# Kernel tuning notes

Measured on AMD Instinct MI355X. Metric: run time of the kernel, lower is better.

The kernel has to match this reference:

```python
import jax, jax.numpy as jnp
import numpy as np

B, V_PREV, V_NEXT = 1, 16384, 65536
F_IN, F_OUT = 512, 256
NNZ_UP, N_EDGE = 65536, 524288
EPS = 1e-5


def batch_spmm(row, col, val, m, x):
    # sparse [m, n] (COO row/col/val) @ dense x [B, n, d] -> [B, m, d]
    contrib = val[None, :, None] * x[:, col, :]          # [B, nnz, d]
    return jnp.zeros((x.shape[0], m, x.shape[2]), x.dtype).at[:, row, :].add(contrib)


def batchnorm(x, g, b):
    # BatchNorm1d in training mode: stats over (batch, node) per channel
    mu = jnp.mean(x, axis=(0, 1), keepdims=True)
    var = jnp.var(x, axis=(0, 1), keepdims=True)
    return (x - mu) * jax.lax.rsqrt(var + EPS) * g + b


def ecc(x, src, dst, w, Ui_W, Ui_b, Uj_W, Uj_b):
    # edge-conditioned graph conv: out_i = Ui(x_i) + sum_{(j->i)} w_e * Uj(x_j)
    n_nodes = x.shape[1]
    uj = x @ Uj_W + Uj_b                                  # [B, V, Fout]
    msg = w[None, :, None] * uj[:, src, :]                # [B, E, Fout]
    agg = jnp.zeros((x.shape[0], n_nodes, Uj_W.shape[1]), x.dtype).at[:, dst, :].add(msg)
    return x @ Ui_W + Ui_b + agg


def setup_inputs() -> dict:
    key = jax.random.key(0)
    ks = jax.random.split(key, 16)
    s_in = 1.0 / np.sqrt(F_IN)
    s_out = 1.0 / np.sqrt(F_OUT)
    p = {}
    p["x"] = jax.random.normal(ks[0], (B, V_PREV, F_IN), jnp.float32)
    p["up_row"] = jnp.arange(NNZ_UP, dtype=jnp.int32)
    p["up_col"] = jax.random.randint(ks[1], (NNZ_UP,), 0, V_PREV)
    p["up_val"] = jax.random.uniform(ks[2], (NNZ_UP,), jnp.float32)
    p["edge_src"] = jax.random.randint(ks[3], (N_EDGE,), 0, V_NEXT)
    p["edge_dst"] = jax.random.randint(ks[4], (N_EDGE,), 0, V_NEXT)
    p["adj_val"] = jax.random.uniform(ks[5], (N_EDGE,), jnp.float32)
    p["W_res"] = jax.random.normal(ks[6], (F_IN, F_OUT), jnp.float32) * s_in
    p["b_res"] = jnp.zeros((F_OUT,), jnp.float32)
    p["bn0_g"] = jnp.ones((F_IN,), jnp.float32)
    p["bn0_b"] = jnp.zeros((F_IN,), jnp.float32)
    p["bn1_g"] = jnp.ones((F_OUT,), jnp.float32)
    p["bn1_b"] = jnp.zeros((F_OUT,), jnp.float32)
    p["Ui0_W"] = jax.random.normal(ks[7], (F_IN, F_OUT), jnp.float32) * s_in
    p["Ui0_b"] = jnp.zeros((F_OUT,), jnp.float32)
    p["Uj0_W"] = jax.random.normal(ks[8], (F_IN, F_OUT), jnp.float32) * s_in
    p["Uj0_b"] = jnp.zeros((F_OUT,), jnp.float32)
    p["Ui1_W"] = jax.random.normal(ks[9], (F_OUT, F_OUT), jnp.float32) * s_out
    p["Ui1_b"] = jnp.zeros((F_OUT,), jnp.float32)
    p["Uj1_W"] = jax.random.normal(ks[10], (F_OUT, F_OUT), jnp.float32) * s_out
    p["Uj1_b"] = jnp.zeros((F_OUT,), jnp.float32)
    return p


def reference(x, up_row, up_col, up_val, edge_src, edge_dst, adj_val,
              W_res, b_res, bn0_g, bn0_b, bn1_g, bn1_b,
              Ui0_W, Ui0_b, Uj0_W, Uj0_b, Ui1_W, Ui1_b, Uj1_W, Uj1_b):
    # residual branch: sparse upsample then 1x1 conv (= linear over channels)
    residual = batch_spmm(up_row, up_col, up_val, V_NEXT, x)      # [B, V_NEXT, F_IN]
    residual = residual @ W_res + b_res                           # [B, V_NEXT, F_OUT]
    # main branch
    out = jax.nn.relu(batchnorm(x, bn0_g, bn0_b))                 # [B, V_PREV, F_IN]
    out = batch_spmm(up_row, up_col, up_val, V_NEXT, out)         # [B, V_NEXT, F_IN]
    out = ecc(out, edge_src, edge_dst, adj_val, Ui0_W, Ui0_b, Uj0_W, Uj0_b)
    out = jax.nn.relu(batchnorm(out, bn1_g, bn1_b))
    out = ecc(out, edge_src, edge_dst, adj_val, Ui1_W, Ui1_b, Uj1_W, Uj1_b)
    return out + residual
```

## Files before the change

### kernel.cpp

```cpp
#include <hip/hip_runtime.h>

#define V_PREV 16384
#define V_NEXT 65536
#define F_IN   512
#define F_OUT  256
#define NNZ_UP 65536
#define N_EDGE 524288

using f32x4 = __attribute__((ext_vector_type(4))) float;
using bfrag = __attribute__((ext_vector_type(8))) short;

__device__ __forceinline__ ushort f2bf(float f) {
    union { float f; unsigned u; } v; v.f = f;
    unsigned r = (v.u + 0x7FFFu + ((v.u >> 16) & 1u)) >> 16;
    return (ushort)r;
}
__device__ __forceinline__ float bf2f(ushort h) {
    union { unsigned u; float f; } v; v.u = ((unsigned)h) << 16; return v.f;
}

__global__ void prep_all_kernel(const float* __restrict__ Wres,
                                const float* __restrict__ Ui0W, const float* __restrict__ Uj0W,
                                const float* __restrict__ Ui1W, const float* __restrict__ Uj1W,
                                const float* __restrict__ Ui1b, const float* __restrict__ bres,
                                const int* __restrict__ up_row, const int* __restrict__ up_col,
                                const float* __restrict__ up_val,
                                ushort* __restrict__ WresT, ushort* __restrict__ W0t,
                                ushort* __restrict__ W1cat, float* __restrict__ biasUi,
                                int* __restrict__ colof, float* __restrict__ valof,
                                int* __restrict__ zeroBase)
{
    int b = blockIdx.x, t = threadIdx.x;
    if (b < 1024) {
        int i = b * 256 + t;
        if (i < 256 * 512) {
            int n = i / 512, k = i % 512;
            WresT[i] = f2bf(Wres[k * 256 + n]);
            W1cat[i] = f2bf(k < 256 ? Ui1W[k * 256 + n] : Uj1W[(k - 256) * 256 + n]);
        }
        {
            int n = i / 512, k = i % 512;
            W0t[i] = f2bf(n < 256 ? Uj0W[k * 256 + n] : Ui0W[k * 256 + (n - 256)]);
        }
        if (i < 256) biasUi[i] = Ui1b[i] + bres[i];
    } else if (b < 1280) {
        int k = (b - 1024) * 256 + t;
        int r = up_row[k];
        colof[r] = up_col[k];
        valof[r] = up_val[k];
    } else {
        int i = (b - 1280) * 256 + t;
        zeroBase[i] = 0;
    }
}

__global__ void hist_bn0_kernel(const int* __restrict__ dst,
                                int* __restrict__ cnt,
                                const float* __restrict__ x,
                                float* __restrict__ psum0, float* __restrict__ psq0)
{
    int b = blockIdx.x, t = threadIdx.x;
    if (b < 2048) {
        int e = b * 256 + t;
        atomicAdd(&cnt[dst[e]], 1);
    } else {
        int blk = b - 2048;
        float s0 = 0, s1 = 0, q0 = 0, q1 = 0;
        for (int r = 0; r < 32; r++) {
            size_t base = ((size_t)blk * 32 + r) * 512;
            float a = x[base + t], bb = x[base + t + 256];
            s0 += a; q0 += a * a; s1 += bb; q1 += bb * bb;
        }
        psum0[blk * 512 + t] = s0; psum0[blk * 512 + t + 256] = s1;
        psq0 [blk * 512 + t] = q0; psq0 [blk * 512 + t + 256] = q1;
    }
}

__global__ void scan_block_kernel(const int* __restrict__ cnt, int* __restrict__ offs,
                                  int* __restrict__ bsum)
{
    __shared__ int buf[2][256];
    int t = threadIdx.x;
    int i = blockIdx.x * 256 + t;
    int v = cnt[i];
    int p = 0;
    buf[0][t] = v;
    __syncthreads();
    for (int d = 1; d < 256; d <<= 1) {
        int nv = buf[p][t] + ((t >= d) ? buf[p][t - d] : 0);
        buf[p ^ 1][t] = nv;
        p ^= 1;
        __syncthreads();
    }
    int incl = buf[p][t];
    offs[i] = incl - v;
    if (t == 255) bsum[blockIdx.x] = incl;
}

__global__ void add_offs_bnfin_kernel(int* __restrict__ offs, const int* __restrict__ bsum,
                                      int* __restrict__ cursor,
                                      const float* __restrict__ psum0, const float* __restrict__ psq0,
                                      const float* __restrict__ g0, const float* __restrict__ b0,
                                      float* __restrict__ sc0, float* __restrict__ sh0)
{
    int b = blockIdx.x, t = threadIdx.x;
    if (b < 256) {
        __shared__ int buf[2][256];
        int v = bsum[t];
        int p = 0;
        buf[0][t] = v;
        __syncthreads();
        for (int d = 1; d < 256; d <<= 1) {
            int nv = buf[p][t] + ((t >= d) ? buf[p][t - d] : 0);
            buf[p ^ 1][t] = nv;
            p ^= 1;
            __syncthreads();
        }
        int excl = buf[p][b] - bsum[b];
        int i = b * 256 + t;
        int o = offs[i] + excl;
        offs[i] = o;
        cursor[i] = o;
    } else {
        int vb = b - 256;
        int gw = (vb * 256 + t) >> 6;
        int lane = t & 63;
        float s = 0, q = 0;
        for (int i = lane; i < 512; i += 64) {
            s += psum0[(size_t)i * 512 + gw];
            q += psq0 [(size_t)i * 512 + gw];
        }
#pragma unroll
        for (int d = 32; d > 0; d >>= 1) {
            s += __shfl_xor(s, d);
            q += __shfl_xor(q, d);
        }
        if (lane == 0) {
            float m = s * (1.0f / V_PREV);
            float v = q * (1.0f / V_PREV) - m * m;
            float r = rsqrtf(v + 1e-5f);
            float scale = r * g0[gw];
            sc0[gw] = scale;
            sh0[gw] = b0[gw] - m * scale;
        }
    }
}

__global__ void bn_finish_kernel(const float* __restrict__ psum, const float* __restrict__ psq,
                                 int nblocks, int C, float invN,
                                 const float* __restrict__ g, const float* __restrict__ b,
                                 float* __restrict__ sc, float* __restrict__ sh)
{
    int gw = (blockIdx.x * blockDim.x + threadIdx.x) >> 6;
    int lane = threadIdx.x & 63;
    if (gw >= C) return;
    float s = 0, q = 0;
    for (int i = lane; i < nblocks; i += 64) {
        s += psum[(size_t)i * C + gw];
        q += psq [(size_t)i * C + gw];
    }
#pragma unroll
    for (int d = 32; d > 0; d >>= 1) {
        s += __shfl_xor(s, d);
        q += __shfl_xor(q, d);
    }
    if (lane == 0) {
        float m = s * invN;
        float v = q * invN - m * m;
        float r = rsqrtf(v + 1e-5f);
        float scale = r * g[gw];
        sc[gw] = scale;
        sh[gw] = b[gw] - m * scale;
    }
}

__global__ __launch_bounds__(256)
void fill_gemm0_kernel(const int* __restrict__ src, const int* __restrict__ dst,
                       const float* __restrict__ adjv,
                       const int* __restrict__ colof, const float* __restrict__ valof,
                       int* __restrict__ cursor, int4* __restrict__ E,
                       const float* __restrict__ x,
                       const ushort* __restrict__ WresT, const ushort* __restrict__ W0t,
                       const float* __restrict__ sc0, const float* __restrict__ sh0,
                       ushort* __restrict__ XW, ushort* __restrict__ XNJ,
                       ushort* __restrict__ XNI)
{
    __shared__ ushort As[128 * 32];
    __shared__ ushort Bs[128 * 32];
    __shared__ float s_sc[512], s_sh[512];

    const int tid = threadIdx.x;
    if (blockIdx.x < 2048) {
        int e = blockIdx.x * 256 + tid;
        int d = dst[e];
        int s = src[e];
        float a = adjv[e];
        int p = atomicAdd(&cursor[d], 1);
        int4 v;
        v.x = s;
        v.y = __float_as_int(a);
        v.z = colof[s];
        v.w = __float_as_int(a * valof[s]);
        E[p] = v;
        return;
    }

    const int id   = blockIdx.x - 2048;
    const int xcd  = id & 7;
    const int rest = id >> 3;
    const int slot = rest / 6;
    const int bx   = rest - slot * 6;
    const int by   = slot * 8 + xcd;

    const bool bnmode = bx >= 2;
    const ushort* Bt = bnmode ? W0t : WresT;
    const int btrow = bnmode ? (bx - 2) * 128 : bx * 128;
    ushort* Cout = (bx < 2) ? XW : (bx < 4 ? XNJ : XNI);
    const int colbase = (bx & 1) * 128;
    const int tM = by * 128;

    for (int i = tid; i < 512; i += 256) { s_sc[i] = sc0[i]; s_sh[i] = sh0[i]; }
    __syncthreads();

    const int lane = tid & 63;
    const int wave = tid >> 6;
    const int wm = wave >> 1, wn = wave & 1;
    const int lr = lane & 15, lg = lane >> 4;

    const int ra = tid >> 1;
    const int ua = (tid & 1) * 2;
    const int rb = tid >> 2;
    const int ub = tid & 3;

    f32x4 acc[4][4] = {};

    for (int k0 = 0; k0 < 512; k0 += 32) {
        const float* xp = &x[(size_t)(tM + ra) * 512 + k0 + ua * 8];
        float4 f0 = *(const float4*)(xp);
        float4 f1 = *(const float4*)(xp + 4);
        float4 f2 = *(const float4*)(xp + 8);
        float4 f3 = *(const float4*)(xp + 12);
        float vv[16] = { f0.x,f0.y,f0.z,f0.w, f1.x,f1.y,f1.z,f1.w,
                         f2.x,f2.y,f2.z,f2.w, f3.x,f3.y,f3.z,f3.w };
        ushort hh[16];
        if (bnmode) {
#pragma unroll
            for (int j = 0; j < 16; j++) {
                int c = k0 + ua * 8 + j;
                hh[j] = f2bf(fmaxf(vv[j] * s_sc[c] + s_sh[c], 0.0f));
            }
        } else {
#pragma unroll
            for (int j = 0; j < 16; j++) hh[j] = f2bf(vv[j]);
        }
        *(uint4*)&As[ra * 32 + ((ua    ) ^ (ra & 3)) * 8] = *(uint4*)&hh[0];
        *(uint4*)&As[ra * 32 + ((ua + 1) ^ (ra & 3)) * 8] = *(uint4*)&hh[8];

#pragma unroll
        for (int i = 0; i < 2; i++) {
            int row = rb + i * 64;
            *(uint4*)&Bs[row * 32 + (ub ^ (row & 3)) * 8] =
                *(const uint4*)&Bt[(size_t)(btrow + row) * 512 + k0 + ub * 8];
        }
        __syncthreads();

        bfrag af[4], bfv[4];
#pragma unroll
        for (int mm = 0; mm < 4; mm++) {
            int row = wm * 64 + mm * 16 + lr;
            af[mm] = *(const bfrag*)&As[row * 32 + (lg ^ (row & 3)) * 8];
        }
#pragma unroll
        for (int nn = 0; nn < 4; nn++) {
            int row = wn * 64 + nn * 16 + lr;
            bfv[nn] = *(const bfrag*)&Bs[row * 32 + (lg ^ (row & 3)) * 8];
        }
#pragma unroll
        for (int mm = 0; mm < 4; mm++)
#pragma unroll
            for (int nn = 0; nn < 4; nn++)
                acc[mm][nn] = __builtin_amdgcn_mfma_f32_16x16x32_bf16(af[mm], bfv[nn], acc[mm][nn], 0, 0, 0);
        __syncthreads();
    }

#pragma unroll
    for (int mm = 0; mm < 4; mm++)
#pragma unroll
        for (int nn = 0; nn < 4; nn++)
#pragma unroll
            for (int r = 0; r < 4; r++) {
                int row = tM + wm * 64 + mm * 16 + lg * 4 + r;
                int col = colbase + wn * 64 + nn * 16 + lr;
                Cout[(size_t)row * 256 + col] = f2bf(acc[mm][nn][r]);
            }
}

__global__ __launch_bounds__(256)
void gather0_kernel(const int* __restrict__ offs, const int* __restrict__ cnt,
                    const int4* __restrict__ E,
                    const int* __restrict__ colof, const float* __restrict__ valof,
                    const ushort* __restrict__ XNJ, const ushort* __restrict__ XNI,
                    const float* __restrict__ ui_b, const float* __restrict__ uj_b,
                    ushort* __restrict__ X1, float* __restrict__ sumA,
                    float* __restrict__ psum1s, float* __restrict__ psq1s)
{
    __shared__ float redS[4][256];
    __shared__ float redQ[4][256];

    int wave = threadIdx.x >> 6;
    int lane = threadIdx.x & 63;
    int f = lane * 4;
    float ub0 = ui_b[f + 0], ub1 = ui_b[f + 1], ub2 = ui_b[f + 2], ub3 = ui_b[f + 3];
    float jb0 = uj_b[f + 0], jb1 = uj_b[f + 1], jb2 = uj_b[f + 2], jb3 = uj_b[f + 3];
    float ss0 = 0, ss1 = 0, ss2 = 0, ss3 = 0;
    float qq0 = 0, qq1 = 0, qq2 = 0, qq3 = 0;

    for (int it = 0; it < 8; it++) {
        int d = (blockIdx.x * 8 + it) * 4 + wave;
        int c = colof[d];
        float s = valof[d];
        ushort4 u = *(const ushort4*)&XNI[(size_t)c * 256 + f];
        const ushort* up = (const ushort*)&u;
        float a0 = ub0 + s * bf2f(up[0]);
        float a1 = ub1 + s * bf2f(up[1]);
        float a2 = ub2 + s * bf2f(up[2]);
        float a3 = ub3 + s * bf2f(up[3]);
        float sA = 0;

        int st = offs[d], n = cnt[d];
        for (int e0 = 0; e0 < n; e0 += 4) {
            int4 ev0 = E[st + e0];
            int4 ev1 = (e0 + 1 < n) ? E[st + e0 + 1] : make_int4(0, 0, 0, 0);
            int4 ev2 = (e0 + 2 < n) ? E[st + e0 + 2] : make_int4(0, 0, 0, 0);
            int4 ev3 = (e0 + 3 < n) ? E[st + e0 + 3] : make_int4(0, 0, 0, 0);
            float w0 = __int_as_float(ev0.w), w1 = __int_as_float(ev1.w);
            float w2 = __int_as_float(ev2.w), w3 = __int_as_float(ev3.w);
            sA += __int_as_float(ev0.y) + __int_as_float(ev1.y)
                + __int_as_float(ev2.y) + __int_as_float(ev3.y);
            ushort4 v0 = *(const ushort4*)&XNJ[(size_t)ev0.z * 256 + f];
            ushort4 v1 = *(const ushort4*)&XNJ[(size_t)ev1.z * 256 + f];
            ushort4 v2 = *(const ushort4*)&XNJ[(size_t)ev2.z * 256 + f];
            ushort4 v3 = *(const ushort4*)&XNJ[(size_t)ev3.z * 256 + f];
            const ushort* p0 = (const ushort*)&v0;
            const ushort* p1 = (const ushort*)&v1;
            const ushort* p2 = (const ushort*)&v2;
            const ushort* p3 = (const ushort*)&v3;
            a0 += w0 * bf2f(p0[0]) + w1 * bf2f(p1[0]) + w2 * bf2f(p2[0]) + w3 * bf2f(p3[0]);
            a1 += w0 * bf2f(p0[1]) + w1 * bf2f(p1[1]) + w2 * bf2f(p2[1]) + w3 * bf2f(p3[1]);
            a2 += w0 * bf2f(p0[2]) + w1 * bf2f(p1[2]) + w2 * bf2f(p2[2]) + w3 * bf2f(p3[2]);
            a3 += w0 * bf2f(p0[3]) + w1 * bf2f(p1[3]) + w2 * bf2f(p2[3]) + w3 * bf2f(p3[3]);
        }
        a0 += sA * jb0; a1 += sA * jb1; a2 += sA * jb2; a3 += sA * jb3;
        *(ushort4*)&X1[(size_t)d * 256 + f] =
            make_ushort4(f2bf(a0), f2bf(a1), f2bf(a2), f2bf(a3));
        if (lane == 0) sumA[d] = sA;
        ss0 += a0; ss1 += a1; ss2 += a2; ss3 += a3;
        qq0 += a0 * a0; qq1 += a1 * a1; qq2 += a2 * a2; qq3 += a3 * a3;
    }

    redS[wave][f + 0] = ss0; redS[wave][f + 1] = ss1;
    redS[wave][f + 2] = ss2; redS[wave][f + 3] = ss3;
    redQ[wave][f + 0] = qq0; redQ[wave][f + 1] = qq1;
    redQ[wave][f + 2] = qq2; redQ[wave][f + 3] = qq3;
    __syncthreads();
    int t = threadIdx.x;
    float ssum = redS[0][t] + redS[1][t] + redS[2][t] + redS[3][t];
    float sq   = redQ[0][t] + redQ[1][t] + redQ[2][t] + redQ[3][t];
    int slab = (blockIdx.x & 63) * 256 + t;
    atomicAdd(&psum1s[slab], ssum);
    atomicAdd(&psq1s[slab], sq);
}

__global__ __launch_bounds__(256)
void gather1G_kernel(const int* __restrict__ offs, const int* __restrict__ cnt,
                     const int4* __restrict__ E,
                     const ushort* __restrict__ X1,
                     const float* __restrict__ sc1, const float* __restrict__ sh1,
                     ushort* __restrict__ G)
{
    int d = blockIdx.x * 4 + (threadIdx.x >> 6);
    int f = (threadIdx.x & 63) * 4;
    float4 sc = *(const float4*)&sc1[f];
    float4 sh = *(const float4*)&sh1[f];
    float a0 = 0, a1 = 0, a2 = 0, a3 = 0;

    int st = offs[d], n = cnt[d];
    for (int e0 = 0; e0 < n; e0 += 4) {
        int4 ev0 = E[st + e0];
        int4 ev1 = (e0 + 1 < n) ? E[st + e0 + 1] : make_int4(0, 0, 0, 0);
        int4 ev2 = (e0 + 2 < n) ? E[st + e0 + 2] : make_int4(0, 0, 0, 0);
        int4 ev3 = (e0 + 3 < n) ? E[st + e0 + 3] : make_int4(0, 0, 0, 0);
        float w0 = __int_as_float(ev0.y), w1 = __int_as_float(ev1.y);
        float w2 = __int_as_float(ev2.y), w3 = __int_as_float(ev3.y);
        ushort4 v0 = *(const ushort4*)&X1[(size_t)ev0.x * 256 + f];
        ushort4 v1 = *(const ushort4*)&X1[(size_t)ev1.x * 256 + f];
        ushort4 v2 = *(const ushort4*)&X1[(size_t)ev2.x * 256 + f];
        ushort4 v3 = *(const ushort4*)&X1[(size_t)ev3.x * 256 + f];
        const ushort* p0 = (const ushort*)&v0;
        const ushort* p1 = (const ushort*)&v1;
        const ushort* p2 = (const ushort*)&v2;
        const ushort* p3 = (const ushort*)&v3;
        a0 += w0 * fmaxf(bf2f(p0[0]) * sc.x + sh.x, 0.0f)
            + w1 * fmaxf(bf2f(p1[0]) * sc.x + sh.x, 0.0f)
            + w2 * fmaxf(bf2f(p2[0]) * sc.x + sh.x, 0.0f)
            + w3 * fmaxf(bf2f(p3[0]) * sc.x + sh.x, 0.0f);
        a1 += w0 * fmaxf(bf2f(p0[1]) * sc.y + sh.y, 0.0f)
            + w1 * fmaxf(bf2f(p1[1]) * sc.y + sh.y, 0.0f)
            + w2 * fmaxf(bf2f(p2[1]) * sc.y + sh.y, 0.0f)
            + w3 * fmaxf(bf2f(p3[1]) * sc.y + sh.y, 0.0f);
        a2 += w0 * fmaxf(bf2f(p0[2]) * sc.z + sh.z, 0.0f)
            + w1 * fmaxf(bf2f(p1[2]) * sc.z + sh.z, 0.0f)
            + w2 * fmaxf(bf2f(p2[2]) * sc.z + sh.z, 0.0f)
            + w3 * fmaxf(bf2f(p3[2]) * sc.z + sh.z, 0.0f);
        a3 += w0 * fmaxf(bf2f(p0[3]) * sc.w + sh.w, 0.0f)
            + w1 * fmaxf(bf2f(p1[3]) * sc.w + sh.w, 0.0f)
            + w2 * fmaxf(bf2f(p2[3]) * sc.w + sh.w, 0.0f)
            + w3 * fmaxf(bf2f(p3[3]) * sc.w + sh.w, 0.0f);
    }
    *(ushort4*)&G[(size_t)d * 256 + f] =
        make_ushort4(f2bf(a0), f2bf(a1), f2bf(a2), f2bf(a3));
}

__global__ __launch_bounds__(512, 1)
void gemm_final_kernel(const ushort* __restrict__ X1, const ushort* __restrict__ G,
                       const ushort* __restrict__ W1cat,
                       const float* __restrict__ sc1, const float* __restrict__ sh1,
                       const float* __restrict__ biasUi, const float* __restrict__ uj1_b,
                       const float* __restrict__ sumA,
                       const int* __restrict__ colof, const float* __restrict__ valof,
                       const ushort* __restrict__ XW,
                       float* __restrict__ out)
{
    __shared__ ushort As[256 * 32];
    __shared__ ushort Bs[256 * 32];
    __shared__ float s_sc[256], s_sh[256];

    const int tid = threadIdx.x;
    const int tM = blockIdx.x * 256;

    if (tid < 256) { s_sc[tid] = sc1[tid]; s_sh[tid] = sh1[tid]; }
    __syncthreads();

    const int lane = tid & 63;
    const int wave = tid >> 6;
    const int wm = wave >> 1, wn = wave & 1;
    const int lr = lane & 15, lg = lane >> 4;

    f32x4 acc[4][8] = {};

    for (int k0 = 0; k0 < 512; k0 += 32) {
#pragma unroll
        for (int i = 0; i < 2; i++) {
            int idx = tid + i * 512;
            int row = idx >> 2, u = idx & 3;
            ushort h[8];
            if (k0 < 256) {
                *(uint4*)h = *(const uint4*)&X1[(size_t)(tM + row) * 256 + k0 + u * 8];
#pragma unroll
                for (int j = 0; j < 8; j++) {
                    int c = k0 + u * 8 + j;
                    h[j] = f2bf(fmaxf(bf2f(h[j]) * s_sc[c] + s_sh[c], 0.0f));
                }
            } else {
                *(uint4*)h = *(const uint4*)&G[(size_t)(tM + row) * 256 + (k0 - 256) + u * 8];
            }
            *(uint4*)&As[row * 32 + (u ^ (row & 3)) * 8] = *(uint4*)h;
        }
#pragma unroll
        for (int i = 0; i < 2; i++) {
            int idx = tid + i * 512;
            int row = idx >> 2, u = idx & 3;
            *(uint4*)&Bs[row * 32 + (u ^ (row & 3)) * 8] =
                *(const uint4*)&W1cat[(size_t)row * 512 + k0 + u * 8];
        }
        __syncthreads();

        bfrag af[4], bfv[8];
#pragma unroll
        for (int mm = 0; mm < 4; mm++) {
            int row = wm * 64 + mm * 16 + lr;
            af[mm] = *(const bfrag*)&As[row * 32 + (lg ^ (row & 3)) * 8];
        }
#pragma unroll
        for (int nn = 0; nn < 8; nn++) {
            int row = wn * 128 + nn * 16 + lr;
            bfv[nn] = *(const bfrag*)&Bs[row * 32 + (lg ^ (row & 3)) * 8];
        }
#pragma unroll
        for (int mm = 0; mm < 4; mm++)
#pragma unroll
            for (int nn = 0; nn < 8; nn++)
                acc[mm][nn] = __builtin_amdgcn_mfma_f32_16x16x32_bf16(af[mm], bfv[nn], acc[mm][nn], 0, 0, 0);
        __syncthreads();
    }

    float bUi[8], bUj[8];
#pragma unroll
    for (int nn = 0; nn < 8; nn++) {
        int col = wn * 128 + nn * 16 + lr;
        bUi[nn] = biasUi[col];
        bUj[nn] = uj1_b[col];
    }
#pragma unroll
    for (int mm = 0; mm < 4; mm++) {
#pragma unroll
        for (int r = 0; r < 4; r++) {
            int row = tM + wm * 64 + mm * 16 + lg * 4 + r;
            int c = colof[row];
            float s = valof[row];
            float sA = sumA[row];
#pragma unroll
            for (int nn = 0; nn < 8; nn++) {
                int col = wn * 128 + nn * 16 + lr;
                float v = acc[mm][nn][r] + bUi[nn] + sA * bUj[nn]
                        + s * bf2f(XW[(size_t)c * 256 + col]);
                out[(size_t)row * 256 + col] = v;
            }
        }
    }
}

extern "C" void kernel_launch(void* const* d_in, const int* in_sizes, int n_in,
                              void* d_out, int out_size, void* d_ws, size_t ws_size,
                              hipStream_t stream)
{
    const float* x      = (const float*)d_in[0];
    const int*   up_row = (const int*)  d_in[1];
    const int*   up_col = (const int*)  d_in[2];
    const float* up_val = (const float*)d_in[3];
    const int*   e_src  = (const int*)  d_in[4];
    const int*   e_dst  = (const int*)  d_in[5];
    const float* adjv   = (const float*)d_in[6];
    const float* W_res  = (const float*)d_in[7];
    const float* b_res  = (const float*)d_in[8];
    const float* bn0_g  = (const float*)d_in[9];
    const float* bn0_b  = (const float*)d_in[10];
    const float* bn1_g  = (const float*)d_in[11];
    const float* bn1_b  = (const float*)d_in[12];
    const float* Ui0_W  = (const float*)d_in[13];
    const float* Ui0_b  = (const float*)d_in[14];
    const float* Uj0_W  = (const float*)d_in[15];
    const float* Uj0_b  = (const float*)d_in[16];
    const float* Ui1_W  = (const float*)d_in[17];
    const float* Ui1_b  = (const float*)d_in[18];
    const float* Uj1_W  = (const float*)d_in[19];
    const float* Uj1_b  = (const float*)d_in[20];

    float* out = (float*)d_out;

    char* ws = (char*)d_ws;
    size_t off = 0;
    auto alloc = [&](size_t bytes) -> char* {
        char* p = ws + off;
        off = (off + bytes + 255) & ~(size_t)255;
        return p;
    };
    ushort* XW    = (ushort*)alloc((size_t)V_PREV * F_OUT * 2);
    ushort* XNJ   = (ushort*)alloc((size_t)V_PREV * F_OUT * 2);
    ushort* XNI   = (ushort*)alloc((size_t)V_PREV * F_OUT * 2);
    ushort* X1    = (ushort*)alloc((size_t)V_NEXT * F_OUT * 2);
    ushort* G     = (ushort*)alloc((size_t)V_NEXT * F_OUT * 2);
    int*    cnt   = (int*)   alloc(V_NEXT * 4);
    float*  psum1s= (float*) alloc(64 * 256 * 4);
    float*  psq1s = (float*) alloc(64 * 256 * 4);
    float*  sumA  = (float*) alloc(V_NEXT * 4);
    int*    offs  = (int*)   alloc(V_NEXT * 4);
    int*    cursor= (int*)   alloc(V_NEXT * 4);
    int*    bsum  = (int*)   alloc(256 * 4);
    int4*   E     = (int4*)  alloc((size_t)N_EDGE * 16);
    int*    colof = (int*)   alloc(V_NEXT * 4);
    float*  valof = (float*) alloc(V_NEXT * 4);
    ushort* WresT = (ushort*)alloc(256 * 512 * 2);
    ushort* W0t   = (ushort*)alloc(512 * 512 * 2);
    ushort* W1cat = (ushort*)alloc(256 * 512 * 2);
    float*  biasUi= (float*) alloc(256 * 4);
    float*  psum0 = (float*) alloc(512 * 512 * 4);
    float*  psq0  = (float*) alloc(512 * 512 * 4);
    float*  sc0   = (float*) alloc(512 * 4);
    float*  sh0   = (float*) alloc(512 * 4);
    float*  sc1   = (float*) alloc(256 * 4);
    float*  sh1   = (float*) alloc(256 * 4);
    (void)ws_size; (void)in_sizes; (void)n_in; (void)out_size;

    prep_all_kernel<<<1664, 256, 0, stream>>>(W_res, Ui0_W, Uj0_W, Ui1_W, Uj1_W,
                                              Ui1_b, b_res,
                                              up_row, up_col, up_val,
                                              WresT, W0t, W1cat, biasUi,
                                              colof, valof, cnt);

    hist_bn0_kernel<<<2560, 256, 0, stream>>>(e_dst, cnt, x, psum0, psq0);

    scan_block_kernel<<<256, 256, 0, stream>>>(cnt, offs, bsum);

    add_offs_bnfin_kernel<<<384, 256, 0, stream>>>(offs, bsum, cursor,
                                                   psum0, psq0, bn0_g, bn0_b, sc0, sh0);

    fill_gemm0_kernel<<<2816, 256, 0, stream>>>(e_src, e_dst, adjv, colof, valof,
                                                cursor, E,
                                                x, WresT, W0t, sc0, sh0,
                                                XW, XNJ, XNI);

    gather0_kernel<<<2048, 256, 0, stream>>>(offs, cnt, E, colof, valof,
                                             XNJ, XNI, Ui0_b, Uj0_b,
                                             X1, sumA, psum1s, psq1s);

    bn_finish_kernel<<<64, 256, 0, stream>>>(psum1s, psq1s, 64, 256, 1.0f / V_NEXT,
                                             bn1_g, bn1_b, sc1, sh1);

    gather1G_kernel<<<V_NEXT / 4, 256, 0, stream>>>(offs, cnt, E, X1, sc1, sh1, G);

    gemm_final_kernel<<<256, 512, 0, stream>>>(X1, G, W1cat, sc1, sh1,
                                               biasUi, Uj1_b, sumA,
                                               colof, valof, XW, out);
}
```

Baseline: 238.1 us.

## Merge prep kernels, split edge records, unroll gathers, pad LDS tiles

Merges the prep and histogram/BN0-stats kernels into one launch and replaces the in-kernel zeroing with a memset. Splits each 16-byte edge record into two 8-byte arrays, so gather1G reads only the half it needs. Both gather loops are unrolled to eight edges with all loads issued before any math, to raise memory-level parallelism. The XOR-swizzled LDS layout in the GEMMs is replaced by a padded row stride of 36. The padding may bring back LDS bank conflicts and slightly raises LDS use, and the deeper unroll raises register pressure.

```diff
diff --git a/kernel.cpp b/kernel.cpp
--- a/kernel.cpp
+++ b/kernel.cpp
@@ -10,6 +10,8 @@
 using f32x4 = __attribute__((ext_vector_type(4))) float;
 using bfrag = __attribute__((ext_vector_type(8))) short;
 
+#define LSTR 36
+
 __device__ __forceinline__ ushort f2bf(float f) {
     union { float f; unsigned u; } v; v.f = f;
     unsigned r = (v.u + 0x7FFFu + ((v.u >> 16) & 1u)) >> 16;
@@ -19,16 +21,19 @@
     union { unsigned u; float f; } v; v.u = ((unsigned)h) << 16; return v.f;
 }
 
-__global__ void prep_all_kernel(const float* __restrict__ Wres,
-                                const float* __restrict__ Ui0W, const float* __restrict__ Uj0W,
-                                const float* __restrict__ Ui1W, const float* __restrict__ Uj1W,
-                                const float* __restrict__ Ui1b, const float* __restrict__ bres,
-                                const int* __restrict__ up_row, const int* __restrict__ up_col,
-                                const float* __restrict__ up_val,
-                                ushort* __restrict__ WresT, ushort* __restrict__ W0t,
-                                ushort* __restrict__ W1cat, float* __restrict__ biasUi,
-                                int* __restrict__ colof, float* __restrict__ valof,
-                                int* __restrict__ zeroBase)
+__global__ void mega_prep_kernel(const float* __restrict__ Wres,
+                                 const float* __restrict__ Ui0W, const float* __restrict__ Uj0W,
+                                 const float* __restrict__ Ui1W, const float* __restrict__ Uj1W,
+                                 const float* __restrict__ Ui1b, const float* __restrict__ bres,
+                                 const int* __restrict__ up_row, const int* __restrict__ up_col,
+                                 const float* __restrict__ up_val,
+                                 const int* __restrict__ dst,
+                                 const float* __restrict__ x,
+                                 ushort* __restrict__ WresT, ushort* __restrict__ W0t,
+                                 ushort* __restrict__ W1cat, float* __restrict__ biasUi,
+                                 int* __restrict__ colof, float* __restrict__ valof,
+                                 int* __restrict__ cnt,
+                                 float* __restrict__ psum0, float* __restrict__ psq0)
 {
     int b = blockIdx.x, t = threadIdx.x;
     if (b < 1024) {
@@ -48,23 +53,11 @@
         int r = up_row[k];
         colof[r] = up_col[k];
         valof[r] = up_val[k];
-    } else {
-        int i = (b - 1280) * 256 + t;
-        zeroBase[i] = 0;
-    }
-}
-
-__global__ void hist_bn0_kernel(const int* __restrict__ dst,
-                                int* __restrict__ cnt,
-                                const float* __restrict__ x,
-                                float* __restrict__ psum0, float* __restrict__ psq0)
-{
-    int b = blockIdx.x, t = threadIdx.x;
-    if (b < 2048) {
-        int e = b * 256 + t;
+    } else if (b < 3328) {
+        int e = (b - 1280) * 256 + t;
         atomicAdd(&cnt[dst[e]], 1);
     } else {
-        int blk = b - 2048;
+        int blk = b - 3328;
         float s0 = 0, s1 = 0, q0 = 0, q1 = 0;
         for (int r = 0; r < 32; r++) {
             size_t base = ((size_t)blk * 32 + r) * 512;
@@ -178,15 +171,16 @@
 void fill_gemm0_kernel(const int* __restrict__ src, const int* __restrict__ dst,
                        const float* __restrict__ adjv,
                        const int* __restrict__ colof, const float* __restrict__ valof,
-                       int* __restrict__ cursor, int4* __restrict__ E,
+                       int* __restrict__ cursor,
+                       int2* __restrict__ E0, int2* __restrict__ E1,
                        const float* __restrict__ x,
                        const ushort* __restrict__ WresT, const ushort* __restrict__ W0t,
                        const float* __restrict__ sc0, const float* __restrict__ sh0,
                        ushort* __restrict__ XW, ushort* __restrict__ XNJ,
                        ushort* __restrict__ XNI)
 {
-    __shared__ ushort As[128 * 32];
-    __shared__ ushort Bs[128 * 32];
+    __shared__ ushort As[128 * LSTR];
+    __shared__ ushort Bs[128 * LSTR];
     __shared__ float s_sc[512], s_sh[512];
 
     const int tid = threadIdx.x;
@@ -196,12 +190,8 @@
         int s = src[e];
         float a = adjv[e];
         int p = atomicAdd(&cursor[d], 1);
-        int4 v;
-        v.x = s;
-        v.y = __float_as_int(a);
-        v.z = colof[s];
-        v.w = __float_as_int(a * valof[s]);
-        E[p] = v;
+        E1[p] = make_int2(s, __float_as_int(a));
+        E0[p] = make_int2(colof[s], __float_as_int(a * valof[s]));
         return;
     }
 
@@ -253,13 +243,13 @@
 #pragma unroll
             for (int j = 0; j < 16; j++) hh[j] = f2bf(vv[j]);
         }
-        *(uint4*)&As[ra * 32 + ((ua    ) ^ (ra & 3)) * 8] = *(uint4*)&hh[0];
-        *(uint4*)&As[ra * 32 + ((ua + 1) ^ (ra & 3)) * 8] = *(uint4*)&hh[8];
+        *(uint4*)&As[ra * LSTR + ua * 8]       = *(uint4*)&hh[0];
+        *(uint4*)&As[ra * LSTR + (ua + 1) * 8] = *(uint4*)&hh[8];
 
 #pragma unroll
         for (int i = 0; i < 2; i++) {
             int row = rb + i * 64;
-            *(uint4*)&Bs[row * 32 + (ub ^ (row & 3)) * 8] =
+            *(uint4*)&Bs[row * LSTR + ub * 8] =
                 *(const uint4*)&Bt[(size_t)(btrow + row) * 512 + k0 + ub * 8];
         }
         __syncthreads();
@@ -268,12 +258,12 @@
 #pragma unroll
         for (int mm = 0; mm < 4; mm++) {
             int row = wm * 64 + mm * 16 + lr;
-            af[mm] = *(const bfrag*)&As[row * 32 + (lg ^ (row & 3)) * 8];
+            af[mm] = *(const bfrag*)&As[row * LSTR + lg * 8];
         }
 #pragma unroll
         for (int nn = 0; nn < 4; nn++) {
             int row = wn * 64 + nn * 16 + lr;
-            bfv[nn] = *(const bfrag*)&Bs[row * 32 + (lg ^ (row & 3)) * 8];
+            bfv[nn] = *(const bfrag*)&Bs[row * LSTR + lg * 8];
         }
 #pragma unroll
         for (int mm = 0; mm < 4; mm++)
@@ -297,7 +287,7 @@
 
 __global__ __launch_bounds__(256)
 void gather0_kernel(const int* __restrict__ offs, const int* __restrict__ cnt,
-                    const int4* __restrict__ E,
+                    const int2* __restrict__ E0, const int2* __restrict__ E1,
                     const int* __restrict__ colof, const float* __restrict__ valof,
                     const ushort* __restrict__ XNJ, const ushort* __restrict__ XNI,
                     const float* __restrict__ ui_b, const float* __restrict__ uj_b,
@@ -310,6 +300,7 @@
     int wave = threadIdx.x >> 6;
     int lane = threadIdx.x & 63;
     int f = lane * 4;
+    int fb = f * 2;
     float ub0 = ui_b[f + 0], ub1 = ui_b[f + 1], ub2 = ui_b[f + 2], ub3 = ui_b[f + 3];
     float jb0 = uj_b[f + 0], jb1 = uj_b[f + 1], jb2 = uj_b[f + 2], jb3 = uj_b[f + 3];
     float ss0 = 0, ss1 = 0, ss2 = 0, ss3 = 0;
@@ -319,7 +310,7 @@
         int d = (blockIdx.x * 8 + it) * 4 + wave;
         int c = colof[d];
         float s = valof[d];
-        ushort4 u = *(const ushort4*)&XNI[(size_t)c * 256 + f];
+        ushort4 u = *(const ushort4*)((const char*)XNI + ((c << 9) + fb));
         const ushort* up = (const ushort*)&u;
         float a0 = ub0 + s * bf2f(up[0]);
         float a1 = ub1 + s * bf2f(up[1]);
@@ -328,27 +319,26 @@
         float sA = 0;
 
         int st = offs[d], n = cnt[d];
-        for (int e0 = 0; e0 < n; e0 += 4) {
-            int4 ev0 = E[st + e0];
-            int4 ev1 = (e0 + 1 < n) ? E[st + e0 + 1] : make_int4(0, 0, 0, 0);
-            int4 ev2 = (e0 + 2 < n) ? E[st + e0 + 2] : make_int4(0, 0, 0, 0);
-            int4 ev3 = (e0 + 3 < n) ? E[st + e0 + 3] : make_int4(0, 0, 0, 0);
-            float w0 = __int_as_float(ev0.w), w1 = __int_as_float(ev1.w);
-            float w2 = __int_as_float(ev2.w), w3 = __int_as_float(ev3.w);
-            sA += __int_as_float(ev0.y) + __int_as_float(ev1.y)
-                + __int_as_float(ev2.y) + __int_as_float(ev3.y);
-            ushort4 v0 = *(const ushort4*)&XNJ[(size_t)ev0.z * 256 + f];
-            ushort4 v1 = *(const ushort4*)&XNJ[(size_t)ev1.z * 256 + f];
-            ushort4 v2 = *(const ushort4*)&XNJ[(size_t)ev2.z * 256 + f];
-            ushort4 v3 = *(const ushort4*)&XNJ[(size_t)ev3.z * 256 + f];
-            const ushort* p0 = (const ushort*)&v0;
-            const ushort* p1 = (const ushort*)&v1;
-            const ushort* p2 = (const ushort*)&v2;
-            const ushort* p3 = (const ushort*)&v3;
-            a0 += w0 * bf2f(p0[0]) + w1 * bf2f(p1[0]) + w2 * bf2f(p2[0]) + w3 * bf2f(p3[0]);
-            a1 += w0 * bf2f(p0[1]) + w1 * bf2f(p1[1]) + w2 * bf2f(p2[1]) + w3 * bf2f(p3[1]);
-            a2 += w0 * bf2f(p0[2]) + w1 * bf2f(p1[2]) + w2 * bf2f(p2[2]) + w3 * bf2f(p3[2]);
-            a3 += w0 * bf2f(p0[3]) + w1 * bf2f(p1[3]) + w2 * bf2f(p2[3]) + w3 * bf2f(p3[3]);
+        for (int e0 = 0; e0 < n; e0 += 8) {
+            int2 ev[8], eva[8];
+#pragma unroll
+            for (int j = 0; j < 8; j++) {
+                bool ok = (e0 + j) < n;
+                ev[j]  = ok ? E0[st + e0 + j] : make_int2(0, 0);
+                eva[j] = ok ? E1[st + e0 + j] : make_int2(0, 0);
+            }
+            ushort4 v[8];
+#pragma unroll
+            for (int j = 0; j < 8; j++)
+                v[j] = *(const ushort4*)((const char*)XNJ + ((ev[j].x << 9) + fb));
+#pragma unroll
+            for (int j = 0; j < 8; j++) {
+                float w = __int_as_float(ev[j].y);
+                sA += __int_as_float(eva[j].y);
+                const ushort* p = (const ushort*)&v[j];
+                a0 += w * bf2f(p[0]); a1 += w * bf2f(p[1]);
+                a2 += w * bf2f(p[2]); a3 += w * bf2f(p[3]);
+            }
         }
         a0 += sA * jb0; a1 += sA * jb1; a2 += sA * jb2; a3 += sA * jb3;
         *(ushort4*)&X1[(size_t)d * 256 + f] =
@@ -373,49 +363,37 @@
 
 __global__ __launch_bounds__(256)
 void gather1G_kernel(const int* __restrict__ offs, const int* __restrict__ cnt,
-                     const int4* __restrict__ E,
+                     const int2* __restrict__ E1,
                      const ushort* __restrict__ X1,
                      const float* __restrict__ sc1, const float* __restrict__ sh1,
                      ushort* __restrict__ G)
 {
     int d = blockIdx.x * 4 + (threadIdx.x >> 6);
     int f = (threadIdx.x & 63) * 4;
+    int fb = f * 2;
     float4 sc = *(const float4*)&sc1[f];
     float4 sh = *(const float4*)&sh1[f];
     float a0 = 0, a1 = 0, a2 = 0, a3 = 0;
 
     int st = offs[d], n = cnt[d];
-    for (int e0 = 0; e0 < n; e0 += 4) {
-        int4 ev0 = E[st + e0];
-        int4 ev1 = (e0 + 1 < n) ? E[st + e0 + 1] : make_int4(0, 0, 0, 0);
-        int4 ev2 = (e0 + 2 < n) ? E[st + e0 + 2] : make_int4(0, 0, 0, 0);
-        int4 ev3 = (e0 + 3 < n) ? E[st + e0 + 3] : make_int4(0, 0, 0, 0);
-        float w0 = __int_as_float(ev0.y), w1 = __int_as_float(ev1.y);
-        float w2 = __int_as_float(ev2.y), w3 = __int_as_float(ev3.y);
-        ushort4 v0 = *(const ushort4*)&X1[(size_t)ev0.x * 256 + f];
-        ushort4 v1 = *(const ushort4*)&X1[(size_t)ev1.x * 256 + f];
-        ushort4 v2 = *(const ushort4*)&X1[(size_t)ev2.x * 256 + f];
-        ushort4 v3 = *(const ushort4*)&X1[(size_t)ev3.x * 256 + f];
-        const ushort* p0 = (const ushort*)&v0;
-        const ushort* p1 = (const ushort*)&v1;
-        const ushort* p2 = (const ushort*)&v2;
-        const ushort* p3 = (const ushort*)&v3;
-        a0 += w0 * fmaxf(bf2f(p0[0]) * sc.x + sh.x, 0.0f)
-            + w1 * fmaxf(bf2f(p1[0]) * sc.x + sh.x, 0.0f)
-            + w2 * fmaxf(bf2f(p2[0]) * sc.x + sh.x, 0.0f)
-            + w3 * fmaxf(bf2f(p3[0]) * sc.x + sh.x, 0.0f);
-        a1 += w0 * fmaxf(bf2f(p0[1]) * sc.y + sh.y, 0.0f)
-            + w1 * fmaxf(bf2f(p1[1]) * sc.y + sh.y, 0.0f)
-            + w2 * fmaxf(bf2f(p2[1]) * sc.y + sh.y, 0.0f)
-            + w3 * fmaxf(bf2f(p3[1]) * sc.y + sh.y, 0.0f);
-        a2 += w0 * fmaxf(bf2f(p0[2]) * sc.z + sh.z, 0.0f)
-            + w1 * fmaxf(bf2f(p1[2]) * sc.z + sh.z, 0.0f)
-            + w2 * fmaxf(bf2f(p2[2]) * sc.z + sh.z, 0.0f)
-            + w3 * fmaxf(bf2f(p3[2]) * sc.z + sh.z, 0.0f);
-        a3 += w0 * fmaxf(bf2f(p0[3]) * sc.w + sh.w, 0.0f)
-            + w1 * fmaxf(bf2f(p1[3]) * sc.w + sh.w, 0.0f)
-            + w2 * fmaxf(bf2f(p2[3]) * sc.w + sh.w, 0.0f)
-            + w3 * fmaxf(bf2f(p3[3]) * sc.w + sh.w, 0.0f);
+    for (int e0 = 0; e0 < n; e0 += 8) {
+        int2 ev[8];
+#pragma unroll
+        for (int j = 0; j < 8; j++)
+            ev[j] = ((e0 + j) < n) ? E1[st + e0 + j] : make_int2(0, 0);
+        ushort4 v[8];
+#pragma unroll
+        for (int j = 0; j < 8; j++)
+            v[j] = *(const ushort4*)((const char*)X1 + ((ev[j].x << 9) + fb));
+#pragma unroll
+        for (int j = 0; j < 8; j++) {
+            float w = __int_as_float(ev[j].y);
+            const ushort* p = (const ushort*)&v[j];
+            a0 += w * fmaxf(bf2f(p[0]) * sc.x + sh.x, 0.0f);
+            a1 += w * fmaxf(bf2f(p[1]) * sc.y + sh.y, 0.0f);
+            a2 += w * fmaxf(bf2f(p[2]) * sc.z + sh.z, 0.0f);
+            a3 += w * fmaxf(bf2f(p[3]) * sc.w + sh.w, 0.0f);
+        }
     }
     *(ushort4*)&G[(size_t)d * 256 + f] =
         make_ushort4(f2bf(a0), f2bf(a1), f2bf(a2), f2bf(a3));
@@ -431,8 +409,8 @@
                        const ushort* __restrict__ XW,
                        float* __restrict__ out)
 {
-    __shared__ ushort As[256 * 32];
-    __shared__ ushort Bs[256 * 32];
+    __shared__ ushort As[256 * LSTR];
+    __shared__ ushort Bs[256 * LSTR];
     __shared__ float s_sc[256], s_sh[256];
 
     const int tid = threadIdx.x;
@@ -464,13 +442,13 @@
             } else {
                 *(uint4*)h = *(const uint4*)&G[(size_t)(tM + row) * 256 + (k0 - 256) + u * 8];
             }
-            *(uint4*)&As[row * 32 + (u ^ (row & 3)) * 8] = *(uint4*)h;
+            *(uint4*)&As[row * LSTR + u * 8] = *(uint4*)h;
         }
 #pragma unroll
         for (int i = 0; i < 2; i++) {
             int idx = tid + i * 512;
             int row = idx >> 2, u = idx & 3;
-            *(uint4*)&Bs[row * 32 + (u ^ (row & 3)) * 8] =
+            *(uint4*)&Bs[row * LSTR + u * 8] =
                 *(const uint4*)&W1cat[(size_t)row * 512 + k0 + u * 8];
         }
         __syncthreads();
@@ -479,12 +457,12 @@
 #pragma unroll
         for (int mm = 0; mm < 4; mm++) {
             int row = wm * 64 + mm * 16 + lr;
-            af[mm] = *(const bfrag*)&As[row * 32 + (lg ^ (row & 3)) * 8];
+            af[mm] = *(const bfrag*)&As[row * LSTR + lg * 8];
         }
 #pragma unroll
         for (int nn = 0; nn < 8; nn++) {
             int row = wn * 128 + nn * 16 + lr;
-            bfv[nn] = *(const bfrag*)&Bs[row * 32 + (lg ^ (row & 3)) * 8];
+            bfv[nn] = *(const bfrag*)&Bs[row * LSTR + lg * 8];
         }
 #pragma unroll
         for (int mm = 0; mm < 4; mm++)
@@ -567,7 +545,8 @@
     int*    offs  = (int*)   alloc(V_NEXT * 4);
     int*    cursor= (int*)   alloc(V_NEXT * 4);
     int*    bsum  = (int*)   alloc(256 * 4);
-    int4*   E     = (int4*)  alloc((size_t)N_EDGE * 16);
+    int2*   E0    = (int2*)  alloc((size_t)N_EDGE * 8);
+    int2*   E1    = (int2*)  alloc((size_t)N_EDGE * 8);
     int*    colof = (int*)   alloc(V_NEXT * 4);
     float*  valof = (float*) alloc(V_NEXT * 4);
     ushort* WresT = (ushort*)alloc(256 * 512 * 2);
@@ -582,13 +561,14 @@
     float*  sh1   = (float*) alloc(256 * 4);
     (void)ws_size; (void)in_sizes; (void)n_in; (void)out_size;
 
-    prep_all_kernel<<<1664, 256, 0, stream>>>(W_res, Ui0_W, Uj0_W, Ui1_W, Uj1_W,
-                                              Ui1_b, b_res,
-                                              up_row, up_col, up_val,
-                                              WresT, W0t, W1cat, biasUi,
-                                              colof, valof, cnt);
-
-    hist_bn0_kernel<<<2560, 256, 0, stream>>>(e_dst, cnt, x, psum0, psq0);
+    hipMemsetAsync(cnt, 0, (size_t)98304 * 4, stream);
+
+    mega_prep_kernel<<<3840, 256, 0, stream>>>(W_res, Ui0_W, Uj0_W, Ui1_W, Uj1_W,
+                                               Ui1_b, b_res,
+                                               up_row, up_col, up_val,
+                                               e_dst, x,
+                                               WresT, W0t, W1cat, biasUi,
+                                               colof, valof, cnt, psum0, psq0);
 
     scan_block_kernel<<<256, 256, 0, stream>>>(cnt, offs, bsum);
 
@@ -596,18 +576,18 @@
                                                    psum0, psq0, bn0_g, bn0_b, sc0, sh0);
 
     fill_gemm0_kernel<<<2816, 256, 0, stream>>>(e_src, e_dst, adjv, colof, valof,
-                                                cursor, E,
+                                                cursor, E0, E1,
                                                 x, WresT, W0t, sc0, sh0,
                                                 XW, XNJ, XNI);
 
-    gather0_kernel<<<2048, 256, 0, stream>>>(offs, cnt, E, colof, valof,
+    gather0_kernel<<<2048, 256, 0, stream>>>(offs, cnt, E0, E1, colof, valof,
                                              XNJ, XNI, Ui0_b, Uj0_b,
                                              X1, sumA, psum1s, psq1s);
 
     bn_finish_kernel<<<64, 256, 0, stream>>>(psum1s, psq1s, 64, 256, 1.0f / V_NEXT,
                                              bn1_g, bn1_b, sc1, sh1);
 
-    gather1G_kernel<<<V_NEXT / 4, 256, 0, stream>>>(offs, cnt, E, X1, sc1, sh1, G);
+    gather1G_kernel<<<V_NEXT / 4, 256, 0, stream>>>(offs, cnt, E1, X1, sc1, sh1, G);
 
     gemm_final_kernel<<<256, 512, 0, stream>>>(X1, G, W1cat, sc1, sh1,
                                                biasUi, Uj1_b, sumA,
```

New measurement: 272.6 us. 14.5% more time.
